# Kernel optimization log

Measured on AMD Instinct MI355X. Metric: run time of the kernel, lower is better.

Reference implementation:

```python
import jax, jax.numpy as jnp
import numpy as np


def setup_inputs() -> dict:
    key = jax.random.key(0)
    k1, k2, k3, k4, k5 = jax.random.split(key, 5)
    B, Tq, Tk, Q, K, U = 8, 32, 2048, 256, 256, 256
    s = 1.0 / np.sqrt(U)
    return {
        "query": jax.random.normal(k1, (B, Tq, Q), dtype=jnp.float32),
        "keys": jax.random.normal(k2, (B, Tk, K), dtype=jnp.float32),
        "Wq": jax.random.normal(k3, (U, Q), dtype=jnp.float32) * s,
        "Wk": jax.random.normal(k4, (U, K), dtype=jnp.float32) * s,
        "v": jax.random.normal(k5, (U,), dtype=jnp.float32) * s,
    }


def reference(query, keys, Wq, Wk, v):
    # Bahdanau additive attention (batch_first, normalize=False)
    # q_proj: [B, Tq, U], k_proj: [B, Tk, U]
    q_proj = jnp.einsum("bqd,ud->bqu", query, Wq)
    k_proj = jnp.einsum("bkd,ud->bku", keys, Wk)
    # additive score: tanh(q + k) . v -> [B, Tq, Tk]
    sum_qk = jnp.tanh(q_proj[:, :, None, :] + k_proj[:, None, :, :])
    scores = jnp.einsum("bqku,u->bqk", sum_qk, v)
    attn = jax.nn.softmax(scores, axis=-1)  # over encoder time Tk
    # weighted sum of encoder states (keys double as values, as in GNMT)
    context = jnp.einsum("bqk,bkd->bqd", attn, keys)
    return context, attn
```

## Files before the change

kernel.cpp:

```cpp
#include <hip/hip_runtime.h>
#include <hip/hip_bf16.h>

#define SCALE_2LOG2E 2.8853900817779268f
#define LOG2E 1.4426950408889634f

#define NB 8
#define TQ 32
#define TK 2048
#define DD 256

typedef unsigned short u16;
typedef u16 u16x8 __attribute__((ext_vector_type(8)));
typedef __bf16 bf16x8 __attribute__((ext_vector_type(8)));
typedef float f32x4 __attribute__((ext_vector_type(4)));

__device__ __forceinline__ u16 f2bf_u(float x) {
  unsigned int xi = __builtin_bit_cast(unsigned int, x);
  unsigned int r = (xi + 0x7fffu + ((xi >> 16) & 1u)) >> 16;
  return (u16)r;
}
__device__ __forceinline__ float bf2f(u16 u) {
  return __builtin_bit_cast(float, (unsigned int)u << 16);
}

__global__ __launch_bounds__(256) void convert_kernel(
    const float* __restrict__ Wk, const float* __restrict__ Wq,
    u16* __restrict__ wkh, u16* __restrict__ wkl,
    u16* __restrict__ wqh, u16* __restrict__ wql) {
  const int bx = blockIdx.x;
  const float* src; u16 *dh, *dl; int base;
  if (bx < 32) { src = Wk; dh = wkh; dl = wkl; base = 0; }
  else         { src = Wq; dh = wqh; dl = wql; base = 32; }
  const int chunk = (bx - base) * 256 + threadIdx.x;
  const float4* s4 = (const float4*)(src + chunk * 8);
  float4 x0 = s4[0], x1 = s4[1];
  const float xs[8] = {x0.x, x0.y, x0.z, x0.w, x1.x, x1.y, x1.z, x1.w};
  u16x8 h, l;
#pragma unroll
  for (int i = 0; i < 8; ++i) {
    u16 hh = f2bf_u(xs[i]);
    h[i] = hh;
    l[i] = f2bf_u(xs[i] - bf2f(hh));
  }
  *(u16x8*)(dh + chunk * 8) = h;
  *(u16x8*)(dl + chunk * 8) = l;
}

__global__ __launch_bounds__(512) void proj_fused(
    const float* __restrict__ keys, const float* __restrict__ query,
    const u16* __restrict__ wkh, const u16* __restrict__ wkl,
    const u16* __restrict__ wqh, const u16* __restrict__ wql,
    float* __restrict__ ekpo, float* __restrict__ eqpo) {
  __shared__ u16 Ah[64 * 64], Al[64 * 64];
  __shared__ u16 Bh[256 * 64], Bl[256 * 64];
  const int tid = threadIdx.x, lane = tid & 63, wv = tid >> 6;
  const int bx = blockIdx.x;
  const float* A; const u16 *bhg, *blg; float* C; int m0;
  if (bx < 256) { A = keys;  bhg = wkh; blg = wkl; C = ekpo; m0 = bx * 64; }
  else          { A = query; bhg = wqh; blg = wql; C = eqpo; m0 = (bx - 256) * 64; }
  const int wr = (wv >> 2) * 32, wc = (wv & 3) * 64;

  const int arow = tid >> 3, ac = tid & 7;
  const float* ag = A + (m0 + arow) * 256 + ac * 8;
  const int aoff = arow * 64 + ((ac ^ (arow & 7)) << 3);

  f32x4 acc[2][4];
#pragma unroll
  for (int i = 0; i < 2; ++i)
#pragma unroll
    for (int j = 0; j < 4; ++j) acc[i][j] = {0.f, 0.f, 0.f, 0.f};

  for (int ks = 0; ks < 4; ++ks) {
    const int k0 = ks * 64;
    float4 a0 = *(const float4*)(ag + k0);
    float4 a1 = *(const float4*)(ag + k0 + 4);
    u16x8 sbh[4], sbl[4];
    int boff[4];
#pragma unroll
    for (int j = 0; j < 4; ++j) {
      int idx = tid + j * 512;
      int row = idx >> 3, c = idx & 7;
      sbh[j] = *(const u16x8*)(bhg + row * 256 + k0 + c * 8);
      sbl[j] = *(const u16x8*)(blg + row * 256 + k0 + c * 8);
      boff[j] = row * 64 + ((c ^ (row & 7)) << 3);
    }
    const float as[8] = {a0.x, a0.y, a0.z, a0.w, a1.x, a1.y, a1.z, a1.w};
    u16x8 hA, lA;
#pragma unroll
    for (int i = 0; i < 8; ++i) {
      u16 hh = f2bf_u(as[i]);
      hA[i] = hh;
      lA[i] = f2bf_u(as[i] - bf2f(hh));
    }
    if (ks) __syncthreads();
    *(u16x8*)&Ah[aoff] = hA;
    *(u16x8*)&Al[aoff] = lA;
#pragma unroll
    for (int j = 0; j < 4; ++j) {
      *(u16x8*)&Bh[boff[j]] = sbh[j];
      *(u16x8*)&Bl[boff[j]] = sbl[j];
    }
    __syncthreads();
#pragma unroll
    for (int s = 0; s < 2; ++s) {
      const int kc = s * 4 + (lane >> 4);
      bf16x8 fa[2][2], fb[4][2];
#pragma unroll
      for (int mh = 0; mh < 2; ++mh) {
        int ra = wr + mh * 16 + (lane & 15);
        int off = ra * 64 + ((kc ^ (ra & 7)) << 3);
        fa[mh][0] = __builtin_bit_cast(bf16x8, *(const u16x8*)&Ah[off]);
        fa[mh][1] = __builtin_bit_cast(bf16x8, *(const u16x8*)&Al[off]);
      }
#pragma unroll
      for (int nh = 0; nh < 4; ++nh) {
        int rb = wc + nh * 16 + (lane & 15);
        int off = rb * 64 + ((kc ^ (rb & 7)) << 3);
        fb[nh][0] = __builtin_bit_cast(bf16x8, *(const u16x8*)&Bh[off]);
        fb[nh][1] = __builtin_bit_cast(bf16x8, *(const u16x8*)&Bl[off]);
      }
#pragma unroll
      for (int mh = 0; mh < 2; ++mh)
#pragma unroll
        for (int nh = 0; nh < 4; ++nh) {
          acc[mh][nh] = __builtin_amdgcn_mfma_f32_16x16x32_bf16(fa[mh][0], fb[nh][0], acc[mh][nh], 0, 0, 0);
          acc[mh][nh] = __builtin_amdgcn_mfma_f32_16x16x32_bf16(fa[mh][0], fb[nh][1], acc[mh][nh], 0, 0, 0);
          acc[mh][nh] = __builtin_amdgcn_mfma_f32_16x16x32_bf16(fa[mh][1], fb[nh][0], acc[mh][nh], 0, 0, 0);
        }
    }
  }
#pragma unroll
  for (int mh = 0; mh < 2; ++mh)
#pragma unroll
    for (int nh = 0; nh < 4; ++nh)
#pragma unroll
      for (int j = 0; j < 4; ++j) {
        int row = m0 + wr + mh * 16 + (lane >> 4) * 4 + j;
        int col = wc + nh * 16 + (lane & 15);
        C[row * 256 + col] = __builtin_amdgcn_exp2f(acc[mh][nh][j] * SCALE_2LOG2E);
      }
}

__global__ __launch_bounds__(1024) void score_ctx_kernel(
    const float* __restrict__ ekp, const float* __restrict__ eqp,
    const float* __restrict__ v, const float* __restrict__ keys,
    float* __restrict__ pbuf, float* __restrict__ part) {
  __shared__ float ek[64 * 256];
  __shared__ float kbuf[64 * 256];
  const int tid = threadIdx.x;
  const int b = blockIdx.y;
  const int kc = blockIdx.x;
  const int kbase = kc * 64;
#pragma unroll
  for (int i = 0; i < 4; ++i) {
    int idx4 = tid + i * 1024;
    int kk = idx4 >> 6, u4 = idx4 & 63;
    float4 t = *(const float4*)(ekp + (b * TK + kbase + kk) * 256 + u4 * 4);
    *(float4*)&ek[kk * 256 + ((u4 ^ (kk & 7)) << 2)] = t;
    float4 kv = *(const float4*)(keys + (b * TK + kbase + kk) * 256 + u4 * 4);
    *(float4*)&kbuf[kk * 256 + u4 * 4] = kv;
  }
  const int lane = tid & 63;
  float vs = (v[lane] + v[lane + 64]) + (v[lane + 128] + v[lane + 192]);
#pragma unroll
  for (int off = 32; off; off >>= 1) vs += __shfl_xor(vs, off, 64);
  __syncthreads();

  const int wv = tid >> 6;
  const int xorv = lane & 7;
  const float* eq0 = eqp + (b * TQ + wv * 2) * 256;
  const float* eq1 = eq0 + 256;
  float a00 = 0.f, a01 = 0.f, a10 = 0.f, a11 = 0.f;
#pragma unroll 4
  for (int u4 = 0; u4 < 64; ++u4) {
    float4 ekv = *(const float4*)&ek[lane * 256 + ((u4 ^ xorv) << 2)];
    float4 qa = *(const float4*)(eq0 + u4 * 4);
    float4 qb = *(const float4*)(eq1 + u4 * 4);
    float4 vv = *(const float4*)(v + u4 * 4);
    float A0 = fmaf(ekv.x, qa.x, 1.f);
    float A1 = fmaf(ekv.y, qa.y, 1.f);
    float A2 = fmaf(ekv.z, qa.z, 1.f);
    float A3 = fmaf(ekv.w, qa.w, 1.f);
    float n01 = fmaf(vv.x, A1, vv.y * A0);
    float n23 = fmaf(vv.z, A3, vv.w * A2);
    a00 = fmaf(n01, __builtin_amdgcn_rcpf(A0 * A1), a00);
    a01 = fmaf(n23, __builtin_amdgcn_rcpf(A2 * A3), a01);
    float B0 = fmaf(ekv.x, qb.x, 1.f);
    float B1 = fmaf(ekv.y, qb.y, 1.f);
    float B2 = fmaf(ekv.z, qb.z, 1.f);
    float B3 = fmaf(ekv.w, qb.w, 1.f);
    float m01 = fmaf(vv.x, B1, vv.y * B0);
    float m23 = fmaf(vv.z, B3, vv.w * B2);
    a10 = fmaf(m01, __builtin_amdgcn_rcpf(B0 * B1), a10);
    a11 = fmaf(m23, __builtin_amdgcn_rcpf(B2 * B3), a11);
  }
  float sc0 = fmaf(-2.f, a00 + a01, vs);
  float sc1 = fmaf(-2.f, a10 + a11, vs);
  float p0 = __builtin_amdgcn_exp2f(sc0 * LOG2E);
  float p1 = __builtin_amdgcn_exp2f(sc1 * LOG2E);
  const int row0 = b * TQ + wv * 2;
  pbuf[row0 * TK + kbase + lane] = p0;
  pbuf[(row0 + 1) * TK + kbase + lane] = p1;

  float4 o0 = {0.f, 0.f, 0.f, 0.f}, o1 = {0.f, 0.f, 0.f, 0.f};
  const int ip0 = __builtin_bit_cast(int, p0);
  const int ip1 = __builtin_bit_cast(int, p1);
#pragma unroll 8
  for (int k = 0; k < 64; ++k) {
    float4 kv = *(const float4*)&kbuf[k * 256 + lane * 4];
    float pk0 = __builtin_bit_cast(float, __builtin_amdgcn_readlane(ip0, k));
    float pk1 = __builtin_bit_cast(float, __builtin_amdgcn_readlane(ip1, k));
    o0.x = fmaf(pk0, kv.x, o0.x); o0.y = fmaf(pk0, kv.y, o0.y);
    o0.z = fmaf(pk0, kv.z, o0.z); o0.w = fmaf(pk0, kv.w, o0.w);
    o1.x = fmaf(pk1, kv.x, o1.x); o1.y = fmaf(pk1, kv.y, o1.y);
    o1.z = fmaf(pk1, kv.z, o1.z); o1.w = fmaf(pk1, kv.w, o1.w);
  }
  float* prow = part + (b * 32 + kc) * 8192 + (wv * 2) * 256 + lane * 4;
  *(float4*)prow = o0;
  *(float4*)(prow + 256) = o1;
}

__global__ __launch_bounds__(256) void combine_kernel(
    const float* __restrict__ part, const float* __restrict__ pbuf,
    float* __restrict__ ctx, float* __restrict__ attn) {
  const int row = blockIdx.x;
  const int b = row >> 5, q = row & 31;
  const int tid = threadIdx.x;
  const float4* p4 = (const float4*)(pbuf + row * TK);
  float4 x0 = p4[tid], x1 = p4[tid + 256];
  float s = ((x0.x + x0.y) + (x0.z + x0.w)) + ((x1.x + x1.y) + (x1.z + x1.w));
#pragma unroll
  for (int off = 32; off; off >>= 1) s += __shfl_xor(s, off, 64);
  __shared__ float reds[4];
  __shared__ float sInvL;
  const int lane = tid & 63, wv = tid >> 6;
  if (lane == 0) reds[wv] = s;
  __syncthreads();
  if (tid == 0) {
    float L = (reds[0] + reds[1]) + (reds[2] + reds[3]);
    sInvL = __builtin_amdgcn_rcpf(L);
  }
  __syncthreads();
  const float invL = sInvL;
  float4* a4 = (float4*)(attn + row * TK);
  a4[tid] = make_float4(x0.x * invL, x0.y * invL, x0.z * invL, x0.w * invL);
  a4[tid + 256] = make_float4(x1.x * invL, x1.y * invL, x1.z * invL, x1.w * invL);
  const float* p = part + b * 32 * 8192 + q * 256 + tid;
  float c0 = 0.f, c1 = 0.f, c2 = 0.f, c3 = 0.f;
#pragma unroll
  for (int kc = 0; kc < 8; ++kc) {
    c0 += p[(kc * 4 + 0) * 8192];
    c1 += p[(kc * 4 + 1) * 8192];
    c2 += p[(kc * 4 + 2) * 8192];
    c3 += p[(kc * 4 + 3) * 8192];
  }
  ctx[row * 256 + tid] = ((c0 + c1) + (c2 + c3)) * invL;
}

extern "C" void kernel_launch(void* const* d_in, const int* in_sizes, int n_in,
                              void* d_out, int out_size, void* d_ws, size_t ws_size,
                              hipStream_t stream) {
  const float* query = (const float*)d_in[0];
  const float* keys  = (const float*)d_in[1];
  const float* Wq    = (const float*)d_in[2];
  const float* Wk    = (const float*)d_in[3];
  const float* v     = (const float*)d_in[4];

  float* out  = (float*)d_out;
  float* ctx  = out;
  float* attn = out + 65536;

  float* ws   = (float*)d_ws;
  float* ekp  = ws;
  float* eqp  = ws + 4194304;
  float* pbuf = ws + 4259840;
  float* part = ws + 4784128;
  u16* u   = (u16*)(ws + 6881280);
  u16* wkh = u;
  u16* wkl = wkh + 65536;
  u16* wqh = wkl + 65536;
  u16* wql = wqh + 65536;

  convert_kernel<<<64, 256, 0, stream>>>(Wk, Wq, wkh, wkl, wqh, wql);
  proj_fused<<<260, 512, 0, stream>>>(keys, query, wkh, wkl, wqh, wql, ekp, eqp);
  score_ctx_kernel<<<dim3(32, 8), 1024, 0, stream>>>(ekp, eqp, v, keys, pbuf, part);
  combine_kernel<<<256, 256, 0, stream>>>(part, pbuf, ctx, attn);
}
```

Before: 56.81 us.

## Split score kernel over query halves and reuse one shared buffer

The score/context kernel now launches twice as many 512-thread blocks, with each block handling 16 queries instead of 32. Shared memory drops from 128KB to 64KB because the projected-key tile and the raw-key tile are staged one after the other in a single buffer, separated by barriers. The aim is more resident blocks per CU and better latency hiding. In exchange, every key tile and projected-key tile is loaded from global memory twice, once per query half, and the keys load is serialized after the score phase.

```diff
diff --git a/kernel.cpp b/kernel.cpp
--- a/kernel.cpp
+++ b/kernel.cpp
@@ -141,24 +141,22 @@
       }
 }
 
-__global__ __launch_bounds__(1024) void score_ctx_kernel(
+__global__ __launch_bounds__(512) void score_ctx_kernel(
     const float* __restrict__ ekp, const float* __restrict__ eqp,
     const float* __restrict__ v, const float* __restrict__ keys,
     float* __restrict__ pbuf, float* __restrict__ part) {
-  __shared__ float ek[64 * 256];
-  __shared__ float kbuf[64 * 256];
+  __shared__ float sbuf[64 * 256];
   const int tid = threadIdx.x;
   const int b = blockIdx.y;
   const int kc = blockIdx.x;
+  const int qh = blockIdx.z;
   const int kbase = kc * 64;
 #pragma unroll
-  for (int i = 0; i < 4; ++i) {
-    int idx4 = tid + i * 1024;
+  for (int i = 0; i < 8; ++i) {
+    int idx4 = tid + i * 512;
     int kk = idx4 >> 6, u4 = idx4 & 63;
     float4 t = *(const float4*)(ekp + (b * TK + kbase + kk) * 256 + u4 * 4);
-    *(float4*)&ek[kk * 256 + ((u4 ^ (kk & 7)) << 2)] = t;
-    float4 kv = *(const float4*)(keys + (b * TK + kbase + kk) * 256 + u4 * 4);
-    *(float4*)&kbuf[kk * 256 + u4 * 4] = kv;
+    *(float4*)&sbuf[kk * 256 + ((u4 ^ (kk & 7)) << 2)] = t;
   }
   const int lane = tid & 63;
   float vs = (v[lane] + v[lane + 64]) + (v[lane + 128] + v[lane + 192]);
@@ -167,13 +165,14 @@
   __syncthreads();
 
   const int wv = tid >> 6;
+  const int q0 = qh * 16 + wv * 2;
   const int xorv = lane & 7;
-  const float* eq0 = eqp + (b * TQ + wv * 2) * 256;
+  const float* eq0 = eqp + (b * TQ + q0) * 256;
   const float* eq1 = eq0 + 256;
   float a00 = 0.f, a01 = 0.f, a10 = 0.f, a11 = 0.f;
 #pragma unroll 4
   for (int u4 = 0; u4 < 64; ++u4) {
-    float4 ekv = *(const float4*)&ek[lane * 256 + ((u4 ^ xorv) << 2)];
+    float4 ekv = *(const float4*)&sbuf[lane * 256 + ((u4 ^ xorv) << 2)];
     float4 qa = *(const float4*)(eq0 + u4 * 4);
     float4 qb = *(const float4*)(eq1 + u4 * 4);
     float4 vv = *(const float4*)(v + u4 * 4);
@@ -198,16 +197,26 @@
   float sc1 = fmaf(-2.f, a10 + a11, vs);
   float p0 = __builtin_amdgcn_exp2f(sc0 * LOG2E);
   float p1 = __builtin_amdgcn_exp2f(sc1 * LOG2E);
-  const int row0 = b * TQ + wv * 2;
+  const int row0 = b * TQ + q0;
   pbuf[row0 * TK + kbase + lane] = p0;
   pbuf[(row0 + 1) * TK + kbase + lane] = p1;
+
+  __syncthreads();
+#pragma unroll
+  for (int i = 0; i < 8; ++i) {
+    int idx4 = tid + i * 512;
+    int kk = idx4 >> 6, d4 = idx4 & 63;
+    float4 kv = *(const float4*)(keys + (b * TK + kbase + kk) * 256 + d4 * 4);
+    *(float4*)&sbuf[kk * 256 + d4 * 4] = kv;
+  }
+  __syncthreads();
 
   float4 o0 = {0.f, 0.f, 0.f, 0.f}, o1 = {0.f, 0.f, 0.f, 0.f};
   const int ip0 = __builtin_bit_cast(int, p0);
   const int ip1 = __builtin_bit_cast(int, p1);
 #pragma unroll 8
   for (int k = 0; k < 64; ++k) {
-    float4 kv = *(const float4*)&kbuf[k * 256 + lane * 4];
+    float4 kv = *(const float4*)&sbuf[k * 256 + lane * 4];
     float pk0 = __builtin_bit_cast(float, __builtin_amdgcn_readlane(ip0, k));
     float pk1 = __builtin_bit_cast(float, __builtin_amdgcn_readlane(ip1, k));
     o0.x = fmaf(pk0, kv.x, o0.x); o0.y = fmaf(pk0, kv.y, o0.y);
@@ -215,7 +224,7 @@
     o1.x = fmaf(pk1, kv.x, o1.x); o1.y = fmaf(pk1, kv.y, o1.y);
     o1.z = fmaf(pk1, kv.z, o1.z); o1.w = fmaf(pk1, kv.w, o1.w);
   }
-  float* prow = part + (b * 32 + kc) * 8192 + (wv * 2) * 256 + lane * 4;
+  float* prow = part + (b * 32 + kc) * 8192 + q0 * 256 + lane * 4;
   *(float4*)prow = o0;
   *(float4*)(prow + 256) = o1;
 }
@@ -283,6 +292,6 @@
 
   convert_kernel<<<64, 256, 0, stream>>>(Wk, Wq, wkh, wkl, wqh, wql);
   proj_fused<<<260, 512, 0, stream>>>(keys, query, wkh, wkl, wqh, wql, ekp, eqp);
-  score_ctx_kernel<<<dim3(32, 8), 1024, 0, stream>>>(ekp, eqp, v, keys, pbuf, part);
+  score_ctx_kernel<<<dim3(32, 8, 2), 512, 0, stream>>>(ekp, eqp, v, keys, pbuf, part);
   combine_kernel<<<256, 256, 0, stream>>>(part, pbuf, ctx, attn);
 }
```

Measured after the change: 56.98 us. Within noise of the previous version (+0.3%).
